# Optimization experiments

Hardware: AMD Instinct MI355X
Metric: run time of the kernel (lower is better)

The kernel has to match this reference:

```python
import jax, jax.numpy as jnp
import numpy as np

B, H, SQ, SK, D = 2, 16, 2048, 2048, 128
SCALE = 0.20884964425119185
P_DROP = 0.125

def setup_inputs() -> dict:
    key = jax.random.key(0)
    k1, k2, k3 = jax.random.split(key, 3)
    x1 = jax.random.normal(k1, (B, H, SQ, D), dtype=jnp.float32)
    x2 = jax.random.normal(k2, (B, H, SK, D), dtype=jnp.float32)
    # inverted dropout mask: 0 with prob p, else 1/(1-p)
    keep = jax.random.uniform(k3, (B, H, SQ, SK)) >= P_DROP
    dropout_mask = keep.astype(jnp.float32) / (1.0 - P_DROP)
    return {"x1": x1, "x2": x2, "dropout_mask": dropout_mask}

def reference(x1, x2, dropout_mask):
    # scores: [B,H,Sq,Sk]
    scores = jnp.einsum('bhqd,bhkd->bhqk', x1, x2) * SCALE
    attn = jax.nn.softmax(scores, axis=-1)
    attn = attn * dropout_mask
    # output: [B,H,Sq,D]
    return jnp.einsum('bhqk,bhkd->bhqd', attn, x2)
```

## Files before the change

### kernel.cpp

```cpp
#include <hip/hip_runtime.h>
#include <hip/hip_bf16.h>

#define SQ 2048
#define SK 2048
#define DD 128
#define NBH 32
#define QBLK 64
#define KBLK 32
#define NKT (SK / KBLK)
#define SCALE 0.20884964425119185f
#define SCL2 (SCALE * 1.4426950408889634f)

typedef __attribute__((ext_vector_type(8))) short short8;
typedef __attribute__((ext_vector_type(4))) float f32x4;

#define KPITCH 272
#define VPITCH 80
#define VOFF 8704
#define SMEM_BYTES 18944

static __device__ __forceinline__ unsigned int pk_bf16(float lo, float hi) {
    float2 f2; f2.x = lo; f2.y = hi;
    __hip_bfloat162 h = __float22bfloat162_rn(f2);
    union { __hip_bfloat162 h2; unsigned int u; } cv; cv.h2 = h;
    return cv.u;
}

#define SOFTMAX_PACK(PA, SA_, SB_, MCa, MCb, LPART)                            \
  { float p_[8];                                                               \
    p_[0] = __builtin_amdgcn_exp2f(SA_[0]*SCL2);                               \
    p_[1] = __builtin_amdgcn_exp2f(SA_[1]*SCL2);                               \
    p_[2] = __builtin_amdgcn_exp2f(SA_[2]*SCL2);                               \
    p_[3] = __builtin_amdgcn_exp2f(SA_[3]*SCL2);                               \
    p_[4] = __builtin_amdgcn_exp2f(SB_[0]*SCL2);                               \
    p_[5] = __builtin_amdgcn_exp2f(SB_[1]*SCL2);                               \
    p_[6] = __builtin_amdgcn_exp2f(SB_[2]*SCL2);                               \
    p_[7] = __builtin_amdgcn_exp2f(SB_[3]*SCL2);                               \
    LPART += ((p_[0]+p_[1]) + (p_[2]+p_[3])) + ((p_[4]+p_[5]) + (p_[6]+p_[7]));\
    p_[0]*=MCa.x; p_[1]*=MCa.y; p_[2]*=MCa.z; p_[3]*=MCa.w;                    \
    p_[4]*=MCb.x; p_[5]*=MCb.y; p_[6]*=MCb.z; p_[7]*=MCb.w;                    \
    unsigned int P0 = pk_bf16(p_[0],p_[1]), P1 = pk_bf16(p_[2],p_[3]);         \
    unsigned int P2 = pk_bf16(p_[4],p_[5]), P3 = pk_bf16(p_[6],p_[7]);         \
    unsigned int a0 = __shfl((int)P0, sA), a2 = __shfl((int)P2, sA);           \
    unsigned int b0 = __shfl((int)P1, sA), b2 = __shfl((int)P3, sA);           \
    unsigned int c0 = __shfl((int)P0, sB), c2 = __shfl((int)P2, sB);           \
    unsigned int d0 = __shfl((int)P1, sB), d2 = __shfl((int)P3, sB);           \
    union { unsigned int u[4]; short8 v; } pb_;                                \
    pb_.u[0] = hi ? a2 : a0; pb_.u[1] = hi ? b2 : b0;                          \
    pb_.u[2] = hi ? c2 : c0; pb_.u[3] = hi ? d2 : d0;                          \
    PA = pb_.v; }

#define BAR()                                                                  \
    asm volatile("s_waitcnt lgkmcnt(0)" ::: "memory");                         \
    __builtin_amdgcn_sched_barrier(0);                                         \
    __builtin_amdgcn_s_barrier();                                              \
    __builtin_amdgcn_sched_barrier(0);

#define BODY_BF(KC0,KC1,VC0,VC1, MC0,MC1, KN0,KN1,VN0,VN1, MN0,MN1, KT)        \
  { const int kbn = ((KT) < NKT - 1) ? ((KT) + 1) * KBLK : (KT) * KBLK;        \
    KN0 = *(const short8*)(x2bb + (size_t)(kbn + kk)      * DD + kd0);         \
    KN1 = *(const short8*)(x2bb + (size_t)(kbn + kk + 16) * DD + kd0);         \
    VN0 = *(const short8*)(x2bb + (size_t)(kbn + 2*kp)     * DD + vdb);        \
    VN1 = *(const short8*)(x2bb + (size_t)(kbn + 2*kp + 1) * DD + vdb);        \
    MN0 = *(const float4*)(mq0 + kbn);                                         \
    MN1 = *(const float4*)(mq0 + kbn + 16);                                    \
    *(short8*)(smem + (kk)      * KPITCH + 2*kd0) = KC0;                       \
    *(short8*)(smem + (kk + 16) * KPITCH + 2*kd0) = KC1;                       \
    { union { short8 s; unsigned int u[4]; } a_, b_;                           \
      a_.s = VC0; b_.s = VC1;                                                  \
      _Pragma("unroll")                                                        \
      for (int j = 0; j < 8; ++j) {                                            \
        unsigned int w = (j & 1)                                               \
            ? ((a_.u[j>>1] >> 16) | (b_.u[j>>1] & 0xffff0000u))                \
            : ((a_.u[j>>1] & 0xffffu) | (b_.u[j>>1] << 16));                   \
        *(unsigned int*)(smem + VOFF + (vdb + j) * VPITCH + 4*kp) = w;         \
      } }                                                                      \
    BAR()                                                                      \
    f32x4 s00={0,0,0,0}, s01={0,0,0,0};                                        \
    __builtin_amdgcn_s_setprio(1);                                             \
    _Pragma("unroll")                                                          \
    for (int ks = 0; ks < 4; ++ks) {                                           \
      short8 ka0 = *(const short8*)(smem + (c)      * KPITCH + ks*64 + 16*g);  \
      short8 ka1 = *(const short8*)(smem + (16 + c) * KPITCH + ks*64 + 16*g);  \
      s00 = __builtin_amdgcn_mfma_f32_16x16x32_bf16(ka0, qf[ks], s00, 0,0,0);  \
      s01 = __builtin_amdgcn_mfma_f32_16x16x32_bf16(ka1, qf[ks], s01, 0,0,0);  \
    }                                                                          \
    __builtin_amdgcn_s_setprio(0);                                             \
    short8 pa;                                                                 \
    SOFTMAX_PACK(pa, s00, s01, MC0, MC1, lp)                                   \
    __builtin_amdgcn_s_setprio(1);                                             \
    _Pragma("unroll")                                                          \
    for (int d8 = 0; d8 < 8; ++d8) {                                           \
      short8 vv = *(const short8*)(smem + VOFF + (d8*16 + c)*VPITCH + 16*g);   \
      o[d8] = __builtin_amdgcn_mfma_f32_16x16x32_bf16(pa, vv, o[d8], 0,0,0);   \
    }                                                                          \
    __builtin_amdgcn_s_setprio(0);                                             \
    BAR()                                                                      \
  }

#define KERNEL_PRE()                                                           \
    __shared__ __align__(16) unsigned char smem[SMEM_BYTES];                   \
    const int tid  = threadIdx.x;                                              \
    const int lane = tid & 63, wid = tid >> 6;                                 \
    const int c = lane & 15, g = lane >> 4;                                    \
    const int bid = blockIdx.x;                                                \
    const int swz = (bid & 7) * 128 + (bid >> 3);  \
    const int bh = swz >> 5;                                                   \
    const int qb = swz & 31;                                                   \
    const float* x1b = x1 + ((size_t)bh * SQ + (size_t)qb * QBLK) * DD;        \
    const float* mb  = mask + ((size_t)bh * SQ + (size_t)qb * QBLK) * SK;      \
    float*      outb = out + ((size_t)bh * SQ + (size_t)qb * QBLK) * DD;       \
    const int sA = c + ((g & 1) << 5);                                         \
    const int sB = sA + 16;                                                    \
    const bool hi = (g >= 2);                                                  \
    const int kk  = tid >> 4, kd0 = (tid & 15) * 8;                            \
    const int kp  = tid & 15, vdb = (tid >> 4) * 8;                            \
    const float* mq0 = mb + (size_t)(wid*16 + c) * SK + 4*g;

#define KERNEL_QLOAD()                                                         \
    short8 qf[4];                                                              \
    {  const float* q0r = x1b + (size_t)(wid*16 + c) * DD;                     \
       _Pragma("unroll")                                                       \
       for (int ks = 0; ks < 4; ++ks) {                                        \
           float4 a = *(const float4*)(q0r + ks*32 + 8*g);                     \
           float4 b = *(const float4*)(q0r + ks*32 + 8*g + 4);                 \
           union { unsigned int u[4]; short8 s; } t;                           \
           t.u[0]=pk_bf16(a.x,a.y); t.u[1]=pk_bf16(a.z,a.w);                   \
           t.u[2]=pk_bf16(b.x,b.y); t.u[3]=pk_bf16(b.z,b.w);                   \
           qf[ks]=t.s;                                                         \
       } }

#define KERNEL_EPILOGUE()                                                      \
    float l = lp; l += __shfl_xor(l, 16); l += __shfl_xor(l, 32);              \
    float il0 = 1.0f/__shfl(l, 4*g+0), il1 = 1.0f/__shfl(l, 4*g+1);            \
    float il2 = 1.0f/__shfl(l, 4*g+2), il3 = 1.0f/__shfl(l, 4*g+3);            \
    float* orow = outb + (size_t)(wid*16) * DD;                                \
    _Pragma("unroll")                                                          \
    for (int d8 = 0; d8 < 8; ++d8) {                                           \
        orow[(4*g + 0) * DD + d8*16 + c] = o[d8][0] * il0;                     \
        orow[(4*g + 1) * DD + d8*16 + c] = o[d8][1] * il1;                     \
        orow[(4*g + 2) * DD + d8*16 + c] = o[d8][2] * il2;                     \
        orow[(4*g + 3) * DD + d8*16 + c] = o[d8][3] * il3;                     \
    }

__global__ __launch_bounds__(256) void cvt_x2(const float* __restrict__ src,
                                              unsigned short* __restrict__ dst,
                                              int n4) {
    int i = blockIdx.x * 256 + threadIdx.x;
    const int stride = gridDim.x * 256;
    for (; i < n4; i += stride) {
        float4 v = ((const float4*)src)[i];
        uint2 w; w.x = pk_bf16(v.x, v.y); w.y = pk_bf16(v.z, v.w);
        ((uint2*)dst)[i] = w;
    }
}

__global__ __launch_bounds__(256, 4) void fattn_bf16(
    const float* __restrict__ x1, const unsigned short* __restrict__ x2b,
    const float* __restrict__ mask, float* __restrict__ out)
{
    KERNEL_PRE()
    const unsigned short* x2bb = x2b + (size_t)bh * SK * DD;

    short8 kA0 = *(const short8*)(x2bb + (size_t)(kk)      * DD + kd0);
    short8 kA1 = *(const short8*)(x2bb + (size_t)(kk + 16) * DD + kd0);
    short8 vA0 = *(const short8*)(x2bb + (size_t)(2*kp)     * DD + vdb);
    short8 vA1 = *(const short8*)(x2bb + (size_t)(2*kp + 1) * DD + vdb);
    float4 mA0 = *(const float4*)(mq0);
    float4 mA1 = *(const float4*)(mq0 + 16);
    short8 kB0, kB1, vB0, vB1; float4 mB0, mB1;

    KERNEL_QLOAD()

    f32x4 o[8] = {};
    float lp = 0.f;

    for (int kt2 = 0; kt2 < NKT / 2; ++kt2) {
        BODY_BF(kA0,kA1,vA0,vA1, mA0,mA1, kB0,kB1,vB0,vB1, mB0,mB1, 2*kt2)
        BODY_BF(kB0,kB1,vB0,vB1, mB0,mB1, kA0,kA1,vA0,vA1, mA0,mA1, 2*kt2 + 1)
    }
    KERNEL_EPILOGUE()
}

#define BODY_F32(KC0,KC1,KC2,KC3, VC0,VC1,VC2,VC3, MC0,MC1,                    \
                 KN0,KN1,KN2,KN3, VN0,VN1,VN2,VN3, MN0,MN1, KT)                \
  { const int kbn = ((KT) < NKT - 1) ? ((KT) + 1) * KBLK : (KT) * KBLK;        \
    KN0 = *(const float4*)(x2fb + (size_t)(kbn + kk)      * DD + kd0);         \
    KN1 = *(const float4*)(x2fb + (size_t)(kbn + kk)      * DD + kd0 + 4);     \
    KN2 = *(const float4*)(x2fb + (size_t)(kbn + kk + 16) * DD + kd0);         \
    KN3 = *(const float4*)(x2fb + (size_t)(kbn + kk + 16) * DD + kd0 + 4);     \
    VN0 = *(const float4*)(x2fb + (size_t)(kbn + 2*kp)     * DD + vdb);        \
    VN1 = *(const float4*)(x2fb + (size_t)(kbn + 2*kp)     * DD + vdb + 4);    \
    VN2 = *(const float4*)(x2fb + (size_t)(kbn + 2*kp + 1) * DD + vdb);        \
    VN3 = *(const float4*)(x2fb + (size_t)(kbn + 2*kp + 1) * DD + vdb + 4);    \
    MN0 = *(const float4*)(mq0 + kbn);                                         \
    MN1 = *(const float4*)(mq0 + kbn + 16);                                    \
    { union { unsigned int u[4]; short8 s; } k0_, k1_;                         \
      k0_.u[0]=pk_bf16(KC0.x,KC0.y); k0_.u[1]=pk_bf16(KC0.z,KC0.w);            \
      k0_.u[2]=pk_bf16(KC1.x,KC1.y); k0_.u[3]=pk_bf16(KC1.z,KC1.w);            \
      k1_.u[0]=pk_bf16(KC2.x,KC2.y); k1_.u[1]=pk_bf16(KC2.z,KC2.w);            \
      k1_.u[2]=pk_bf16(KC3.x,KC3.y); k1_.u[3]=pk_bf16(KC3.z,KC3.w);            \
      *(short8*)(smem + (kk)      * KPITCH + 2*kd0) = k0_.s;                   \
      *(short8*)(smem + (kk + 16) * KPITCH + 2*kd0) = k1_.s; }                 \
    *(unsigned int*)(smem + VOFF + (vdb+0)*VPITCH + 4*kp) = pk_bf16(VC0.x, VC2.x); \
    *(unsigned int*)(smem + VOFF + (vdb+1)*VPITCH + 4*kp) = pk_bf16(VC0.y, VC2.y); \
    *(unsigned int*)(smem + VOFF + (vdb+2)*VPITCH + 4*kp) = pk_bf16(VC0.z, VC2.z); \
    *(unsigned int*)(smem + VOFF + (vdb+3)*VPITCH + 4*kp) = pk_bf16(VC0.w, VC2.w); \
    *(unsigned int*)(smem + VOFF + (vdb+4)*VPITCH + 4*kp) = pk_bf16(VC1.x, VC3.x); \
    *(unsigned int*)(smem + VOFF + (vdb+5)*VPITCH + 4*kp) = pk_bf16(VC1.y, VC3.y); \
    *(unsigned int*)(smem + VOFF + (vdb+6)*VPITCH + 4*kp) = pk_bf16(VC1.z, VC3.z); \
    *(unsigned int*)(smem + VOFF + (vdb+7)*VPITCH + 4*kp) = pk_bf16(VC1.w, VC3.w); \
    BAR()                                                                      \
    f32x4 s00={0,0,0,0}, s01={0,0,0,0};                                        \
    _Pragma("unroll")                                                          \
    for (int ks = 0; ks < 4; ++ks) {                                           \
      short8 ka0 = *(const short8*)(smem + (c)      * KPITCH + ks*64 + 16*g);  \
      short8 ka1 = *(const short8*)(smem + (16 + c) * KPITCH + ks*64 + 16*g);  \
      s00 = __builtin_amdgcn_mfma_f32_16x16x32_bf16(ka0, qf[ks], s00, 0,0,0);  \
      s01 = __builtin_amdgcn_mfma_f32_16x16x32_bf16(ka1, qf[ks], s01, 0,0,0);  \
    }                                                                          \
    short8 pa;                                                                 \
    SOFTMAX_PACK(pa, s00, s01, MC0, MC1, lp)                                   \
    _Pragma("unroll")                                                          \
    for (int d8 = 0; d8 < 8; ++d8) {                                           \
      short8 vv = *(const short8*)(smem + VOFF + (d8*16 + c)*VPITCH + 16*g);   \
      o[d8] = __builtin_amdgcn_mfma_f32_16x16x32_bf16(pa, vv, o[d8], 0,0,0);   \
    }                                                                          \
    BAR()                                                                      \
  }

__global__ __launch_bounds__(256, 3) void fattn_f32(
    const float* __restrict__ x1, const float* __restrict__ x2,
    const float* __restrict__ mask, float* __restrict__ out)
{
    KERNEL_PRE()
    const float* x2fb = x2 + (size_t)bh * SK * DD;

    float4 kA0 = *(const float4*)(x2fb + (size_t)(kk)      * DD + kd0);
    float4 kA1 = *(const float4*)(x2fb + (size_t)(kk)      * DD + kd0 + 4);
    float4 kA2 = *(const float4*)(x2fb + (size_t)(kk + 16) * DD + kd0);
    float4 kA3 = *(const float4*)(x2fb + (size_t)(kk + 16) * DD + kd0 + 4);
    float4 vA0 = *(const float4*)(x2fb + (size_t)(2*kp)     * DD + vdb);
    float4 vA1 = *(const float4*)(x2fb + (size_t)(2*kp)     * DD + vdb + 4);
    float4 vA2 = *(const float4*)(x2fb + (size_t)(2*kp + 1) * DD + vdb);
    float4 vA3 = *(const float4*)(x2fb + (size_t)(2*kp + 1) * DD + vdb + 4);
    float4 mA0 = *(const float4*)(mq0);
    float4 mA1 = *(const float4*)(mq0 + 16);
    float4 kB0,kB1,kB2,kB3, vB0,vB1,vB2,vB3, mB0,mB1;

    KERNEL_QLOAD()

    f32x4 o[8] = {};
    float lp = 0.f;

    for (int kt2 = 0; kt2 < NKT / 2; ++kt2) {
        BODY_F32(kA0,kA1,kA2,kA3, vA0,vA1,vA2,vA3, mA0,mA1,
                 kB0,kB1,kB2,kB3, vB0,vB1,vB2,vB3, mB0,mB1, 2*kt2)
        BODY_F32(kB0,kB1,kB2,kB3, vB0,vB1,vB2,vB3, mB0,mB1,
                 kA0,kA1,kA2,kA3, vA0,vA1,vA2,vA3, mA0,mA1, 2*kt2 + 1)
    }
    KERNEL_EPILOGUE()
}

extern "C" void kernel_launch(void* const* d_in, const int* in_sizes, int n_in,
                              void* d_out, int out_size, void* d_ws, size_t ws_size,
                              hipStream_t stream) {
    const float* x1   = (const float*)d_in[0];
    const float* x2   = (const float*)d_in[1];
    const float* mask = (const float*)d_in[2];
    float* out = (float*)d_out;
    const size_t need = (size_t)NBH * SK * DD * sizeof(unsigned short);
    if (ws_size >= need) {
        unsigned short* x2b = (unsigned short*)d_ws;
        cvt_x2<<<dim3(2048), dim3(256), 0, stream>>>(x2, x2b, NBH*SK*DD/4);
        fattn_bf16<<<dim3(NBH * (SQ / QBLK)), dim3(256), 0, stream>>>(x1, x2b, mask, out);
    } else {
        fattn_f32<<<dim3(NBH * (SQ / QBLK)), dim3(256), 0, stream>>>(x1, x2, mask, out);
    }
}
```

Measured before the change: 184.6 us.

## Load K fragments directly from global and double-buffer V in LDS

In the bf16 path, each wave now reads the K operand for QK^T straight from global memory (bf16 x2) into MFMA registers instead of staging K through LDS. V alone is staged in LDS using two buffers, so the next tile is written after the PV MFMAs and only one barrier per tile is needed instead of two. This cuts LDS traffic and barrier count, but every wave now fetches the same K rows redundantly from global/L2. Global-load latency also lands directly on the MFMA critical path.

```diff
diff --git a/kernel.cpp b/kernel.cpp
--- a/kernel.cpp
+++ b/kernel.cpp
@@ -14,10 +14,13 @@
 typedef __attribute__((ext_vector_type(8))) short short8;
 typedef __attribute__((ext_vector_type(4))) float f32x4;
 
+#define VPITCH 80
+#define V0OFF 0
+#define V1OFF 10240
+#define SMEM_BF 20480
 #define KPITCH 272
-#define VPITCH 80
-#define VOFF 8704
-#define SMEM_BYTES 18944
+#define VOFF_F 8704
+#define SMEM_F32 18944
 
 static __device__ __forceinline__ unsigned int pk_bf16(float lo, float hi) {
     float2 f2; f2.x = lo; f2.y = hi;
@@ -56,32 +59,30 @@
     __builtin_amdgcn_s_barrier();                                              \
     __builtin_amdgcn_sched_barrier(0);
 
-#define BODY_BF(KC0,KC1,VC0,VC1, MC0,MC1, KN0,KN1,VN0,VN1, MN0,MN1, KT)        \
-  { const int kbn = ((KT) < NKT - 1) ? ((KT) + 1) * KBLK : (KT) * KBLK;        \
-    KN0 = *(const short8*)(x2bb + (size_t)(kbn + kk)      * DD + kd0);         \
-    KN1 = *(const short8*)(x2bb + (size_t)(kbn + kk + 16) * DD + kd0);         \
-    VN0 = *(const short8*)(x2bb + (size_t)(kbn + 2*kp)     * DD + vdb);        \
-    VN1 = *(const short8*)(x2bb + (size_t)(kbn + 2*kp + 1) * DD + vdb);        \
-    MN0 = *(const float4*)(mq0 + kbn);                                         \
-    MN1 = *(const float4*)(mq0 + kbn + 16);                                    \
-    *(short8*)(smem + (kk)      * KPITCH + 2*kd0) = KC0;                       \
-    *(short8*)(smem + (kk + 16) * KPITCH + 2*kd0) = KC1;                       \
+#define VSTAGE(VOFF_)                                                          \
     { union { short8 s; unsigned int u[4]; } a_, b_;                           \
-      a_.s = VC0; b_.s = VC1;                                                  \
+      a_.s = vC0; b_.s = vC1;                                                  \
       _Pragma("unroll")                                                        \
       for (int j = 0; j < 8; ++j) {                                            \
         unsigned int w = (j & 1)                                               \
             ? ((a_.u[j>>1] >> 16) | (b_.u[j>>1] & 0xffff0000u))                \
             : ((a_.u[j>>1] & 0xffffu) | (b_.u[j>>1] << 16));                   \
-        *(unsigned int*)(smem + VOFF + (vdb + j) * VPITCH + 4*kp) = w;         \
-      } }                                                                      \
-    BAR()                                                                      \
+        *(unsigned int*)(smem + (VOFF_) + (vdb + j) * VPITCH + 4*kp) = w;      \
+      } }
+
+#define BODY_BF(VOFFc, VOFFn, MC0, MC1, MN0, MN1, KT)                          \
+  { const int kb  = (KT) * KBLK;                                               \
+    const int kbn = (((KT) < NKT - 1) ? (KT) + 1 : (KT)) * KBLK;               \
+    MN0 = *(const float4*)(mq0 + kbn);                                         \
+    MN1 = *(const float4*)(mq0 + kbn + 16);                                    \
+    vC0 = *(const short8*)(x2bb + (size_t)(kbn + 2*kp)     * DD + vdb);        \
+    vC1 = *(const short8*)(x2bb + (size_t)(kbn + 2*kp + 1) * DD + vdb);        \
     f32x4 s00={0,0,0,0}, s01={0,0,0,0};                                        \
     __builtin_amdgcn_s_setprio(1);                                             \
     _Pragma("unroll")                                                          \
     for (int ks = 0; ks < 4; ++ks) {                                           \
-      short8 ka0 = *(const short8*)(smem + (c)      * KPITCH + ks*64 + 16*g);  \
-      short8 ka1 = *(const short8*)(smem + (16 + c) * KPITCH + ks*64 + 16*g);  \
+      short8 ka0 = *(const short8*)(kp0 + (size_t)kb * DD + ks*32);            \
+      short8 ka1 = *(const short8*)(kp1 + (size_t)kb * DD + ks*32);            \
       s00 = __builtin_amdgcn_mfma_f32_16x16x32_bf16(ka0, qf[ks], s00, 0,0,0);  \
       s01 = __builtin_amdgcn_mfma_f32_16x16x32_bf16(ka1, qf[ks], s01, 0,0,0);  \
     }                                                                          \
@@ -91,15 +92,16 @@
     __builtin_amdgcn_s_setprio(1);                                             \
     _Pragma("unroll")                                                          \
     for (int d8 = 0; d8 < 8; ++d8) {                                           \
-      short8 vv = *(const short8*)(smem + VOFF + (d8*16 + c)*VPITCH + 16*g);   \
+      short8 vv = *(const short8*)(smem + (VOFFc) + (d8*16 + c)*VPITCH + 16*g);\
       o[d8] = __builtin_amdgcn_mfma_f32_16x16x32_bf16(pa, vv, o[d8], 0,0,0);   \
     }                                                                          \
     __builtin_amdgcn_s_setprio(0);                                             \
+    VSTAGE(VOFFn)                                                              \
     BAR()                                                                      \
   }
 
-#define KERNEL_PRE()                                                           \
-    __shared__ __align__(16) unsigned char smem[SMEM_BYTES];                   \
+#define KERNEL_PRE(SMEMSZ)                                                     \
+    __shared__ __align__(16) unsigned char smem[SMEMSZ];                       \
     const int tid  = threadIdx.x;                                              \
     const int lane = tid & 63, wid = tid >> 6;                                 \
     const int c = lane & 15, g = lane >> 4;                                    \
@@ -113,7 +115,6 @@
     const int sA = c + ((g & 1) << 5);                                         \
     const int sB = sA + 16;                                                    \
     const bool hi = (g >= 2);                                                  \
-    const int kk  = tid >> 4, kd0 = (tid & 15) * 8;                            \
     const int kp  = tid & 15, vdb = (tid >> 4) * 8;                            \
     const float* mq0 = mb + (size_t)(wid*16 + c) * SK + 4*g;
 
@@ -159,25 +160,28 @@
     const float* __restrict__ x1, const unsigned short* __restrict__ x2b,
     const float* __restrict__ mask, float* __restrict__ out)
 {
-    KERNEL_PRE()
+    KERNEL_PRE(SMEM_BF)
     const unsigned short* x2bb = x2b + (size_t)bh * SK * DD;
-
-    short8 kA0 = *(const short8*)(x2bb + (size_t)(kk)      * DD + kd0);
-    short8 kA1 = *(const short8*)(x2bb + (size_t)(kk + 16) * DD + kd0);
-    short8 vA0 = *(const short8*)(x2bb + (size_t)(2*kp)     * DD + vdb);
-    short8 vA1 = *(const short8*)(x2bb + (size_t)(2*kp + 1) * DD + vdb);
+    const unsigned short* kp0 = x2bb + (size_t)c * DD + 8*g;
+    const unsigned short* kp1 = x2bb + (size_t)(16 + c) * DD + 8*g;
+
+    short8 vC0 = *(const short8*)(x2bb + (size_t)(2*kp)     * DD + vdb);
+    short8 vC1 = *(const short8*)(x2bb + (size_t)(2*kp + 1) * DD + vdb);
     float4 mA0 = *(const float4*)(mq0);
     float4 mA1 = *(const float4*)(mq0 + 16);
-    short8 kB0, kB1, vB0, vB1; float4 mB0, mB1;
+    float4 mB0, mB1;
 
     KERNEL_QLOAD()
+
+    VSTAGE(V0OFF)
+    BAR()
 
     f32x4 o[8] = {};
     float lp = 0.f;
 
     for (int kt2 = 0; kt2 < NKT / 2; ++kt2) {
-        BODY_BF(kA0,kA1,vA0,vA1, mA0,mA1, kB0,kB1,vB0,vB1, mB0,mB1, 2*kt2)
-        BODY_BF(kB0,kB1,vB0,vB1, mB0,mB1, kA0,kA1,vA0,vA1, mA0,mA1, 2*kt2 + 1)
+        BODY_BF(V0OFF, V1OFF, mA0, mA1, mB0, mB1, 2*kt2)
+        BODY_BF(V1OFF, V0OFF, mB0, mB1, mA0, mA1, 2*kt2 + 1)
     }
     KERNEL_EPILOGUE()
 }
@@ -185,10 +189,10 @@
 #define BODY_F32(KC0,KC1,KC2,KC3, VC0,VC1,VC2,VC3, MC0,MC1,                    \
                  KN0,KN1,KN2,KN3, VN0,VN1,VN2,VN3, MN0,MN1, KT)                \
   { const int kbn = ((KT) < NKT - 1) ? ((KT) + 1) * KBLK : (KT) * KBLK;        \
-    KN0 = *(const float4*)(x2fb + (size_t)(kbn + kk)      * DD + kd0);         \
-    KN1 = *(const float4*)(x2fb + (size_t)(kbn + kk)      * DD + kd0 + 4);     \
-    KN2 = *(const float4*)(x2fb + (size_t)(kbn + kk + 16) * DD + kd0);         \
-    KN3 = *(const float4*)(x2fb + (size_t)(kbn + kk + 16) * DD + kd0 + 4);     \
+    KN0 = *(const float4*)(x2fb + (size_t)(kbn + kkf)      * DD + kd0);        \
+    KN1 = *(const float4*)(x2fb + (size_t)(kbn + kkf)      * DD + kd0 + 4);    \
+    KN2 = *(const float4*)(x2fb + (size_t)(kbn + kkf + 16) * DD + kd0);        \
+    KN3 = *(const float4*)(x2fb + (size_t)(kbn + kkf + 16) * DD + kd0 + 4);    \
     VN0 = *(const float4*)(x2fb + (size_t)(kbn + 2*kp)     * DD + vdb);        \
     VN1 = *(const float4*)(x2fb + (size_t)(kbn + 2*kp)     * DD + vdb + 4);    \
     VN2 = *(const float4*)(x2fb + (size_t)(kbn + 2*kp + 1) * DD + vdb);        \
@@ -200,16 +204,16 @@
       k0_.u[2]=pk_bf16(KC1.x,KC1.y); k0_.u[3]=pk_bf16(KC1.z,KC1.w);            \
       k1_.u[0]=pk_bf16(KC2.x,KC2.y); k1_.u[1]=pk_bf16(KC2.z,KC2.w);            \
       k1_.u[2]=pk_bf16(KC3.x,KC3.y); k1_.u[3]=pk_bf16(KC3.z,KC3.w);            \
-      *(short8*)(smem + (kk)      * KPITCH + 2*kd0) = k0_.s;                   \
-      *(short8*)(smem + (kk + 16) * KPITCH + 2*kd0) = k1_.s; }                 \
-    *(unsigned int*)(smem + VOFF + (vdb+0)*VPITCH + 4*kp) = pk_bf16(VC0.x, VC2.x); \
-    *(unsigned int*)(smem + VOFF + (vdb+1)*VPITCH + 4*kp) = pk_bf16(VC0.y, VC2.y); \
-    *(unsigned int*)(smem + VOFF + (vdb+2)*VPITCH + 4*kp) = pk_bf16(VC0.z, VC2.z); \
-    *(unsigned int*)(smem + VOFF + (vdb+3)*VPITCH + 4*kp) = pk_bf16(VC0.w, VC2.w); \
-    *(unsigned int*)(smem + VOFF + (vdb+4)*VPITCH + 4*kp) = pk_bf16(VC1.x, VC3.x); \
-    *(unsigned int*)(smem + VOFF + (vdb+5)*VPITCH + 4*kp) = pk_bf16(VC1.y, VC3.y); \
-    *(unsigned int*)(smem + VOFF + (vdb+6)*VPITCH + 4*kp) = pk_bf16(VC1.z, VC3.z); \
-    *(unsigned int*)(smem + VOFF + (vdb+7)*VPITCH + 4*kp) = pk_bf16(VC1.w, VC3.w); \
+      *(short8*)(smem + (kkf)      * KPITCH + 2*kd0) = k0_.s;                  \
+      *(short8*)(smem + (kkf + 16) * KPITCH + 2*kd0) = k1_.s; }                \
+    *(unsigned int*)(smem + VOFF_F + (vdb+0)*VPITCH + 4*kp) = pk_bf16(VC0.x, VC2.x); \
+    *(unsigned int*)(smem + VOFF_F + (vdb+1)*VPITCH + 4*kp) = pk_bf16(VC0.y, VC2.y); \
+    *(unsigned int*)(smem + VOFF_F + (vdb+2)*VPITCH + 4*kp) = pk_bf16(VC0.z, VC2.z); \
+    *(unsigned int*)(smem + VOFF_F + (vdb+3)*VPITCH + 4*kp) = pk_bf16(VC0.w, VC2.w); \
+    *(unsigned int*)(smem + VOFF_F + (vdb+4)*VPITCH + 4*kp) = pk_bf16(VC1.x, VC3.x); \
+    *(unsigned int*)(smem + VOFF_F + (vdb+5)*VPITCH + 4*kp) = pk_bf16(VC1.y, VC3.y); \
+    *(unsigned int*)(smem + VOFF_F + (vdb+6)*VPITCH + 4*kp) = pk_bf16(VC1.z, VC3.z); \
+    *(unsigned int*)(smem + VOFF_F + (vdb+7)*VPITCH + 4*kp) = pk_bf16(VC1.w, VC3.w); \
     BAR()                                                                      \
     f32x4 s00={0,0,0,0}, s01={0,0,0,0};                                        \
     _Pragma("unroll")                                                          \
@@ -223,7 +227,7 @@
     SOFTMAX_PACK(pa, s00, s01, MC0, MC1, lp)                                   \
     _Pragma("unroll")                                                          \
     for (int d8 = 0; d8 < 8; ++d8) {                                           \
-      short8 vv = *(const short8*)(smem + VOFF + (d8*16 + c)*VPITCH + 16*g);   \
+      short8 vv = *(const short8*)(smem + VOFF_F + (d8*16 + c)*VPITCH + 16*g); \
       o[d8] = __builtin_amdgcn_mfma_f32_16x16x32_bf16(pa, vv, o[d8], 0,0,0);   \
     }                                                                          \
     BAR()                                                                      \
@@ -233,13 +237,14 @@
     const float* __restrict__ x1, const float* __restrict__ x2,
     const float* __restrict__ mask, float* __restrict__ out)
 {
-    KERNEL_PRE()
+    KERNEL_PRE(SMEM_F32)
     const float* x2fb = x2 + (size_t)bh * SK * DD;
-
-    float4 kA0 = *(const float4*)(x2fb + (size_t)(kk)      * DD + kd0);
-    float4 kA1 = *(const float4*)(x2fb + (size_t)(kk)      * DD + kd0 + 4);
-    float4 kA2 = *(const float4*)(x2fb + (size_t)(kk + 16) * DD + kd0);
-    float4 kA3 = *(const float4*)(x2fb + (size_t)(kk + 16) * DD + kd0 + 4);
+    const int kkf = tid >> 4, kd0 = (tid & 15) * 8;
+
+    float4 kA0 = *(const float4*)(x2fb + (size_t)(kkf)      * DD + kd0);
+    float4 kA1 = *(const float4*)(x2fb + (size_t)(kkf)      * DD + kd0 + 4);
+    float4 kA2 = *(const float4*)(x2fb + (size_t)(kkf + 16) * DD + kd0);
+    float4 kA3 = *(const float4*)(x2fb + (size_t)(kkf + 16) * DD + kd0 + 4);
     float4 vA0 = *(const float4*)(x2fb + (size_t)(2*kp)     * DD + vdb);
     float4 vA1 = *(const float4*)(x2fb + (size_t)(2*kp)     * DD + vdb + 4);
     float4 vA2 = *(const float4*)(x2fb + (size_t)(2*kp + 1) * DD + vdb);
```

Result: slower. 381.1 us (+106.5%).
